# Kernel tuning notes

Measured on AMD Instinct MI355X. Metric: run time of the kernel, lower is better.

## Reference

```python
import jax, jax.numpy as jnp
import numpy as np

N = 100000      # total nodes (herb + ingredient + target concatenated)
E = 1600000     # edges (all etypes concatenated)
D_IN = 128
D_HID = 128
D_OUT = 128
BN_EPS = 1e-5
LEAKY_SLOPE = 0.01


def setup_inputs() -> dict:
    key = jax.random.key(0)
    ks = jax.random.split(key, 8)
    x = jax.random.normal(ks[0], (N, D_IN), dtype=jnp.float32)
    src = jax.random.randint(ks[1], (E,), 0, N, dtype=jnp.int32)
    dst = jax.random.randint(ks[2], (E,), 0, N, dtype=jnp.int32)
    W1 = jax.random.normal(ks[3], (D_IN, D_HID), dtype=jnp.float32) * (1.0 / np.sqrt(D_IN))
    b1 = jnp.zeros((D_HID,), jnp.float32)
    W2 = jax.random.normal(ks[4], (D_HID, D_OUT), dtype=jnp.float32) * (1.0 / np.sqrt(D_HID))
    b2 = jnp.zeros((D_OUT,), jnp.float32)
    gamma = jnp.ones((D_HID,), jnp.float32)
    beta = jnp.zeros((D_HID,), jnp.float32)
    run_mean = jax.random.normal(ks[5], (D_HID,), jnp.float32) * 0.1
    run_var = jax.random.uniform(ks[6], (D_HID,), jnp.float32, 0.5, 1.5)
    return {"x": x, "src": src, "dst": dst, "W1": W1, "b1": b1,
            "W2": W2, "b2": b2, "gamma": gamma, "beta": beta,
            "run_mean": run_mean, "run_var": run_var}


def _graph_conv(h, s, d, W, b, norm_src, norm_dst):
    # DGL GraphConv, norm='both': D_out^{-1/2} then sum-aggregate then D_in^{-1/2}, then linear
    h = h * norm_src                                   # [N, d]
    m = jax.ops.segment_sum(h[s], d, num_segments=N)   # gather + spmm-aggregate
    m = m * norm_dst
    return m @ W + b


def reference(x, src, dst, W1, b1, W2, b2, gamma, beta, run_mean, run_var):
    # dgl.add_self_loop: append (i, i) for every node
    loop = jnp.arange(N, dtype=src.dtype)
    s = jnp.concatenate([src, loop])
    d = jnp.concatenate([dst, loop])
    ones = jnp.ones(s.shape[0], jnp.float32)
    out_deg = jnp.maximum(jax.ops.segment_sum(ones, s, num_segments=N), 1.0)
    in_deg = jnp.maximum(jax.ops.segment_sum(ones, d, num_segments=N), 1.0)
    norm_src = (out_deg ** -0.5)[:, None]
    norm_dst = (in_deg ** -0.5)[:, None]

    # layer 0: conv -> BN (eval, running stats) -> leaky_relu -> dropout (eval = identity)
    h = _graph_conv(x, s, d, W1, b1, norm_src, norm_dst)
    h = (h - run_mean) * jax.lax.rsqrt(run_var + BN_EPS) * gamma + beta
    h = jnp.where(h > 0, h, LEAKY_SLOPE * h)

    # layer 1 (last): conv only
    h = _graph_conv(h, s, d, W2, b2, norm_src, norm_dst)
    return h
```

## Files before the change

kernel.cpp:

```cpp
#include <hip/hip_runtime.h>

#define NN 100000
#define NE 1600000
#define D 128
#define LEAKY 0.01f
#define BNEPS 1e-5f

#define GS 128
#define CHUNK 12500
#define B 782
#define BSHIFT 7
#define BMASK 127
#define NSB (B * GS / 256)

typedef short v8s __attribute__((ext_vector_type(8)));
typedef float v4f __attribute__((ext_vector_type(4)));

__device__ __forceinline__ unsigned f2bf(float f) {
    unsigned u = __float_as_uint(f);
    return (u + 0x7fffu + ((u >> 16) & 1u)) >> 16;
}
__device__ __forceinline__ float bf2f(unsigned h) {
    return __uint_as_float(h << 16);
}


__global__ __launch_bounds__(1024) void hist_kernel(const int* __restrict__ src,
                                                    const int* __restrict__ dst,
                                                    int* __restrict__ hist,
                                                    int* __restrict__ hist2) {
    __shared__ int h[B];
    __shared__ int h2[B];
    for (int i = threadIdx.x; i < B; i += 1024) { h[i] = 0; h2[i] = 0; }
    __syncthreads();
    int g = blockIdx.x;
    const int* dp = dst + g * CHUNK;
    const int* sp = src + g * CHUNK;
    for (int k = threadIdx.x; k < CHUNK; k += 1024) {
        atomicAdd(&h[dp[k] >> BSHIFT], 1);
        atomicAdd(&h2[sp[k] >> BSHIFT], 1);
    }
    __syncthreads();
    for (int i = threadIdx.x; i < B; i += 1024) {
        hist[i * GS + g]  = h[i];
        hist2[i * GS + g] = h2[i];
    }
}

__global__ void scanA2(const int* __restrict__ a, const int* __restrict__ a2,
                       int* __restrict__ bsum, int* __restrict__ bsum2) {
    __shared__ int sm[256];
    int t = threadIdx.x;
    bool second = blockIdx.x >= NSB;
    int blk = second ? blockIdx.x - NSB : blockIdx.x;
    const int* sp = second ? a2 : a;
    sm[t] = sp[blk * 256 + t];
    __syncthreads();
    for (int s = 128; s > 0; s >>= 1) {
        if (t < s) sm[t] += sm[t + s];
        __syncthreads();
    }
    if (t == 0) (second ? bsum2 : bsum)[blk] = sm[0];
}

__global__ void scanC2(const int* __restrict__ a, const int* __restrict__ a2,
                       const int* __restrict__ bsum, const int* __restrict__ bsum2,
                       int* __restrict__ offs, int* __restrict__ offs2) {
    __shared__ int sm[256];
    __shared__ int bo;
    int t = threadIdx.x;
    bool second = blockIdx.x >= NSB;
    int blk = second ? blockIdx.x - NSB : blockIdx.x;
    const int* sp = second ? a2 : a;
    const int* bs = second ? bsum2 : bsum;
    int part = 0;
    for (int j = t; j < blk; j += 256) part += bs[j];
    sm[t] = part;
    __syncthreads();
    for (int s = 128; s > 0; s >>= 1) {
        if (t < s) sm[t] += sm[t + s];
        __syncthreads();
    }
    if (t == 0) bo = sm[0];
    __syncthreads();
    int i = blk * 256 + t;
    int v = sp[i];
    sm[t] = v;
    __syncthreads();
    for (int off = 1; off < 256; off <<= 1) {
        int x = (t >= off) ? sm[t - off] : 0;
        __syncthreads();
        sm[t] += x;
        __syncthreads();
    }
    (second ? offs2 : offs)[i] = bo + sm[t] - v;
}

__global__ __launch_bounds__(1024) void sort_kernel(const int* __restrict__ src,
                                                    const int* __restrict__ dst,
                                                    const int* __restrict__ offs,
                                                    const int* __restrict__ offs2,
                                                    unsigned* __restrict__ ebuf,
                                                    unsigned char* __restrict__ sbuf8) {
    __shared__ int cur[B];
    __shared__ int cur2[B];
    int g = blockIdx.x;
    for (int i = threadIdx.x; i < B; i += 1024) {
        cur[i]  = offs[i * GS + g];
        cur2[i] = offs2[i * GS + g];
    }
    __syncthreads();
    const int* sp = src + g * CHUNK;
    const int* dp = dst + g * CHUNK;
    for (int k = threadIdx.x; k < CHUNK; k += 1024) {
        int d = dp[k], s = sp[k];
        int pos = atomicAdd(&cur[d >> BSHIFT], 1);
        ebuf[pos] = ((unsigned)(d & BMASK) << 17) | (unsigned)s;
        int pos2 = atomicAdd(&cur2[s >> BSHIFT], 1);
        sbuf8[pos2] = (unsigned char)(s & BMASK);
    }
}


__global__ __launch_bounds__(256) void bucket_prep(
    const int* __restrict__ offs, const int* __restrict__ offs2,
    unsigned* __restrict__ ebuf, const unsigned char* __restrict__ sbuf8,
    const float* __restrict__ x, int* __restrict__ row,
    float* __restrict__ norm_s, float* __restrict__ norm_d,
    unsigned* __restrict__ hb)
{
    __shared__ int cnt[128];
    __shared__ int sc[128];
    __shared__ float nsm[128];
    const int b = blockIdx.x;
    const int t = threadIdx.x;

    {
        const int s = offs2[b * GS];
        const int e = (b == B - 1) ? NE : offs2[(b + 1) * GS];
        if (t < 128) cnt[t] = 0;
        __syncthreads();
        for (int k = s + t; k < e; k += 256)
            atomicAdd(&cnt[sbuf8[k]], 1);
        __syncthreads();
        if (t < 128) {
            int node = b * 128 + t;
            if (node < NN) {
                float ns = rsqrtf((float)(cnt[t] + 1));
                norm_s[node] = ns;
                nsm[t] = ns;
            }
        }
        __syncthreads();
        for (int idx = t; idx < 128 * 32; idx += 256) {
            int r = idx >> 5, q = idx & 31;
            int node = b * 128 + r;
            if (node >= NN) continue;
            float ns = nsm[r];
            float4 v = ((const float4*)x)[(size_t)node * 32 + q];
            uint2 w;
            w.x = f2bf(v.x * ns) | (f2bf(v.y * ns) << 16);
            w.y = f2bf(v.z * ns) | (f2bf(v.w * ns) << 16);
            *(uint2*)(hb + (size_t)node * 64 + 2 * q) = w;
        }
    }
    __syncthreads();

    {
        const int s = offs[b * GS];
        const int e = (b == B - 1) ? NE : offs[(b + 1) * GS];
        if (t < 128) cnt[t] = 0;
        __syncthreads();

        unsigned ent[16];
        int nent = 0;
        for (int k = s + t; k < e && nent < 16; k += 256) {
            unsigned u = ebuf[k];
            ent[nent++] = u;
            atomicAdd(&cnt[u >> 17], 1);
        }
        __syncthreads();

        if (t < 128) sc[t] = cnt[t];
        __syncthreads();
        for (int off = 1; off < 128; off <<= 1) {
            int v = 0;
            if (t < 128 && t >= off) v = sc[t - off];
            __syncthreads();
            if (t < 128) sc[t] += v;
            __syncthreads();
        }
        if (t < 128) {
            int st = s + sc[t] - cnt[t];
            int node = b * 128 + t;
            if (node < NN) {
                row[node] = st;
                norm_d[node] = rsqrtf((float)(cnt[t] + 1));
            }
            cnt[t] = st;
        }
        if (b == B - 1 && t == 0) row[NN] = NE;
        __syncthreads();

        for (int i = 0; i < nent; ++i) {
            unsigned u = ent[i];
            int pos = atomicAdd(&cnt[u >> 17], 1);
            ebuf[pos] = u & 0x1FFFFu;
        }
    }
}


__global__ __launch_bounds__(256) void csr_agg(
    const int* __restrict__ rowp, const int* __restrict__ csr,
    const unsigned* __restrict__ hp,
    unsigned* __restrict__ Ahi, unsigned* __restrict__ Alo)
{
    int i = blockIdx.x * 4 + (threadIdx.x >> 6);
    if (i >= NN) return;
    const int lane = threadIdx.x & 63;
    const int half = lane >> 5;
    const int c2   = lane & 31;

    float4 acc = {0.f, 0.f, 0.f, 0.f};
    if (half == 0) {
        uint2 u = *(const uint2*)(hp + (size_t)i * 64 + 2 * c2);
        acc.x = __uint_as_float(u.x << 16);
        acc.y = __uint_as_float(u.x & 0xffff0000u);
        acc.z = __uint_as_float(u.y << 16);
        acc.w = __uint_as_float(u.y & 0xffff0000u);
    }

    int start = rowp[i], end = rowp[i + 1];
    for (int base = start; base < end; base += 64) {
        int n = end - base; if (n > 64) n = 64;
        int sv = csr[base + (lane < n ? lane : n - 1)];
        int nfull = n & ~15;
        int j = 0;
        for (; j < nfull; j += 16) {
            int ss[8]; uint2 uu[8];
            #pragma unroll
            for (int t = 0; t < 8; ++t) ss[t] = __shfl(sv, j + 2 * t + half);
            #pragma unroll
            for (int t = 0; t < 8; ++t)
                uu[t] = *(const uint2*)(hp + (size_t)ss[t] * 64 + 2 * c2);
            #pragma unroll
            for (int t = 0; t < 8; ++t) {
                acc.x += __uint_as_float(uu[t].x << 16);
                acc.y += __uint_as_float(uu[t].x & 0xffff0000u);
                acc.z += __uint_as_float(uu[t].y << 16);
                acc.w += __uint_as_float(uu[t].y & 0xffff0000u);
            }
        }
        if (j < n) {
            int ss[8]; uint2 uu[8];
            #pragma unroll
            for (int t = 0; t < 8; ++t) {
                int e = j + 2 * t + half;
                ss[t] = __shfl(sv, e < n ? e : n - 1);
            }
            #pragma unroll
            for (int t = 0; t < 8; ++t)
                uu[t] = *(const uint2*)(hp + (size_t)ss[t] * 64 + 2 * c2);
            #pragma unroll
            for (int t = 0; t < 8; ++t) {
                if (j + 2 * t + half < n) {
                    acc.x += __uint_as_float(uu[t].x << 16);
                    acc.y += __uint_as_float(uu[t].x & 0xffff0000u);
                    acc.z += __uint_as_float(uu[t].y << 16);
                    acc.w += __uint_as_float(uu[t].y & 0xffff0000u);
                }
            }
        }
    }

    acc.x += __shfl_xor(acc.x, 32);
    acc.y += __shfl_xor(acc.y, 32);
    acc.z += __shfl_xor(acc.z, 32);
    acc.w += __shfl_xor(acc.w, 32);

    unsigned h0 = f2bf(acc.x), h1 = f2bf(acc.y);
    unsigned h2 = f2bf(acc.z), h3 = f2bf(acc.w);
    if (half == 0) {
        uint2 w = { h0 | (h1 << 16), h2 | (h3 << 16) };
        *(uint2*)(Ahi + (size_t)i * 64 + 2 * c2) = w;
    } else {
        float l0 = acc.x - bf2f(h0), l1 = acc.y - bf2f(h1);
        float l2 = acc.z - bf2f(h2), l3 = acc.w - bf2f(h3);
        uint2 w = { f2bf(l0) | (f2bf(l1) << 16), f2bf(l2) | (f2bf(l3) << 16) };
        *(uint2*)(Alo + (size_t)i * 64 + 2 * c2) = w;
    }
}


template<bool LAYER0>
__global__ __launch_bounds__(256) void gemm_kernel(
    const unsigned* __restrict__ Ahi_g, const unsigned* __restrict__ Alo_g,
    const float* __restrict__ W, const float* __restrict__ bias,
    const float* __restrict__ norm_s, const float* __restrict__ norm_d,
    const float* __restrict__ gamma, const float* __restrict__ beta,
    const float* __restrict__ rmean, const float* __restrict__ rvar,
    float* __restrict__ outf, unsigned short* __restrict__ outb)
{
    __shared__ unsigned lhi[64 * 68];
    __shared__ unsigned llo[64 * 68];

    const int w    = threadIdx.x >> 6;
    const int lane = threadIdx.x & 63;
    const int quad = lane >> 4;
    const int l16  = lane & 15;

    v8s Bhi[2][4], Blo[2][4];
    int col[2];
    #pragma unroll
    for (int ct = 0; ct < 2; ++ct) {
        col[ct] = 32 * w + 16 * ct + l16;
        #pragma unroll
        for (int q = 0; q < 4; ++q) {
            int kb = 32 * q + quad * 8;
            v8s hi8, lo8;
            #pragma unroll
            for (int kk = 0; kk < 8; ++kk) {
                float wv = W[(kb + kk) * D + col[ct]];
                unsigned h = f2bf(wv);
                hi8[kk] = (short)h;
                lo8[kk] = (short)f2bf(wv - bf2f(h));
            }
            Bhi[ct][q] = hi8;
            Blo[ct][q] = lo8;
        }
    }

    float bcol[2], s[2] = {0.f, 0.f}, sh[2] = {0.f, 0.f};
    #pragma unroll
    for (int ct = 0; ct < 2; ++ct) {
        bcol[ct] = bias[col[ct]];
        if (LAYER0) {
            s[ct]  = gamma[col[ct]] * rsqrtf(rvar[col[ct]] + BNEPS);
            sh[ct] = beta[col[ct]] - rmean[col[ct]] * s[ct];
        }
    }

    for (int row0 = blockIdx.x * 64; row0 < NN; row0 += gridDim.x * 64) {
        __syncthreads();
        for (int idx = threadIdx.x; idx < 64 * 64; idx += 256) {
            int r = idx >> 6, cp = idx & 63;
            int rw = row0 + r;
            unsigned vh = 0, vl = 0;
            if (rw < NN) {
                vh = Ahi_g[(size_t)rw * 64 + cp];
                vl = Alo_g[(size_t)rw * 64 + cp];
            }
            lhi[r * 68 + cp] = vh;
            llo[r * 68 + cp] = vl;
        }
        __syncthreads();

        #pragma unroll
        for (int rt = 0; rt < 4; ++rt) {
            v4f acc0 = {0.f, 0.f, 0.f, 0.f};
            v4f acc1 = {0.f, 0.f, 0.f, 0.f};
            #pragma unroll
            for (int q = 0; q < 4; ++q) {
                const unsigned short* ph = (const unsigned short*)lhi
                    + (rt * 16 + l16) * 136 + q * 32 + quad * 8;
                const unsigned short* pl = (const unsigned short*)llo
                    + (rt * 16 + l16) * 136 + q * 32 + quad * 8;
                v8s ahi = *(const v8s*)ph;
                v8s alo = *(const v8s*)pl;
                acc0 = __builtin_amdgcn_mfma_f32_16x16x32_bf16(ahi, Bhi[0][q], acc0, 0, 0, 0);
                acc0 = __builtin_amdgcn_mfma_f32_16x16x32_bf16(alo, Bhi[0][q], acc0, 0, 0, 0);
                acc0 = __builtin_amdgcn_mfma_f32_16x16x32_bf16(ahi, Blo[0][q], acc0, 0, 0, 0);
                acc1 = __builtin_amdgcn_mfma_f32_16x16x32_bf16(ahi, Bhi[1][q], acc1, 0, 0, 0);
                acc1 = __builtin_amdgcn_mfma_f32_16x16x32_bf16(alo, Bhi[1][q], acc1, 0, 0, 0);
                acc1 = __builtin_amdgcn_mfma_f32_16x16x32_bf16(ahi, Blo[1][q], acc1, 0, 0, 0);
            }
            #pragma unroll
            for (int r = 0; r < 4; ++r) {
                int rw = row0 + rt * 16 + quad * 4 + r;
                if (rw >= NN) continue;
                float nd = norm_d[rw];
                float o0 = acc0[r] * nd + bcol[0];
                float o1 = acc1[r] * nd + bcol[1];
                if (LAYER0) {
                    o0 = o0 * s[0] + sh[0];
                    o1 = o1 * s[1] + sh[1];
                    o0 = o0 > 0.f ? o0 : LEAKY * o0;
                    o1 = o1 > 0.f ? o1 : LEAKY * o1;
                    float ns = norm_s[rw];
                    o0 *= ns; o1 *= ns;
                    outb[(size_t)rw * D + col[0]] = (unsigned short)f2bf(o0);
                    outb[(size_t)rw * D + col[1]] = (unsigned short)f2bf(o1);
                } else {
                    outf[(size_t)rw * D + col[0]] = o0;
                    outf[(size_t)rw * D + col[1]] = o1;
                }
            }
        }
    }
}


extern "C" void kernel_launch(void* const* d_in, const int* in_sizes, int n_in,
                              void* d_out, int out_size, void* d_ws, size_t ws_size,
                              hipStream_t stream) {
    const float* x     = (const float*)d_in[0];
    const int*   src   = (const int*)d_in[1];
    const int*   dst   = (const int*)d_in[2];
    const float* W1    = (const float*)d_in[3];
    const float* b1    = (const float*)d_in[4];
    const float* W2    = (const float*)d_in[5];
    const float* b2    = (const float*)d_in[6];
    const float* gamma = (const float*)d_in[7];
    const float* beta  = (const float*)d_in[8];
    const float* rmean = (const float*)d_in[9];
    const float* rvar  = (const float*)d_in[10];
    float* out = (float*)d_out;

    unsigned* hb = (unsigned*)d_out;

    unsigned* Ahi   = (unsigned*)d_ws;
    unsigned* Alo   = Ahi + (size_t)NN * 64;
    float*    norm  = (float*)(Alo + (size_t)NN * 64);
    int*      aux   = (int*)(norm + 2 * NN);
    int*      hist  = aux + NN;
    int*      offs  = hist + B * GS;
    int*      bsum  = offs + B * GS;
    int*      boffs = bsum + B;
    unsigned* ebuf  = (unsigned*)(boffs + B);
    float* norm_s = norm;
    float* norm_d = norm + NN;
    int*   row    = hist;
    int*   bsum2  = aux;

    int*           hist2 = (int*)Ahi;
    int*           offs2 = hist2 + B * GS;
    unsigned char* sbuf8 = (unsigned char*)(offs2 + B * GS);

    hist_kernel<<<GS, 1024, 0, stream>>>(src, dst, hist, hist2);
    scanA2<<<2 * NSB, 256, 0, stream>>>(hist, hist2, bsum, bsum2);
    scanC2<<<2 * NSB, 256, 0, stream>>>(hist, hist2, bsum, bsum2, offs, offs2);
    sort_kernel<<<GS, 1024, 0, stream>>>(src, dst, offs, offs2, ebuf, sbuf8);
    bucket_prep<<<B, 256, 0, stream>>>(offs, offs2, ebuf, sbuf8, x, row,
                                       norm_s, norm_d, hb);

    const int AGG_BLOCKS = (NN + 3) / 4;
    const int GEMM_BLOCKS = 784;
    csr_agg<<<AGG_BLOCKS, 256, 0, stream>>>(row, (const int*)ebuf, hb, Ahi, Alo);
    gemm_kernel<true><<<GEMM_BLOCKS, 256, 0, stream>>>(Ahi, Alo, W1, b1,
                                                       norm_s, norm_d,
                                                       gamma, beta, rmean, rvar,
                                                       nullptr, (unsigned short*)hb);
    csr_agg<<<AGG_BLOCKS, 256, 0, stream>>>(row, (const int*)ebuf, hb, Ahi, Alo);
    gemm_kernel<false><<<GEMM_BLOCKS, 256, 0, stream>>>(Ahi, Alo, W2, b2,
                                                        norm_s, norm_d,
                                                        nullptr, nullptr, nullptr, nullptr,
                                                        out, nullptr);
}
```

Baseline: 399.2 us.

## Stage bucket scatter through LDS-local sort for coalesced global writes

The edge bucketing kernel now counts bucket sizes per chunk, builds local prefix sums in shared memory, scatters edges into an LDS buffer, then writes them out to global memory in bucket-contiguous runs located by binary search. The group count is doubled and the chunk halved so the local buffers fit in shared memory. This aims to replace scattered single-element global writes with more contiguous ones. In exchange it adds extra passes, two 1024-wide scans with many barriers, and a binary search per element.

```diff
diff --git a/kernel.cpp b/kernel.cpp
--- a/kernel.cpp
+++ b/kernel.cpp
@@ -6,8 +6,8 @@
 #define LEAKY 0.01f
 #define BNEPS 1e-5f
 
-#define GS 128
-#define CHUNK 12500
+#define GS 256
+#define CHUNK 6250
 #define B 782
 #define BSHIFT 7
 #define BMASK 127
@@ -96,28 +96,83 @@
     (second ? offs2 : offs)[i] = bo + sm[t] - v;
 }
 
+
 __global__ __launch_bounds__(1024) void sort_kernel(const int* __restrict__ src,
                                                     const int* __restrict__ dst,
                                                     const int* __restrict__ offs,
                                                     const int* __restrict__ offs2,
                                                     unsigned* __restrict__ ebuf,
                                                     unsigned char* __restrict__ sbuf8) {
-    __shared__ int cur[B];
+    __shared__ unsigned      lbuf[CHUNK];
+    __shared__ unsigned char lbuf2[CHUNK];
+    __shared__ int lst [B + 1];
+    __shared__ int lst2[B + 1];
+    __shared__ int cur [B];
     __shared__ int cur2[B];
-    int g = blockIdx.x;
-    for (int i = threadIdx.x; i < B; i += 1024) {
-        cur[i]  = offs[i * GS + g];
-        cur2[i] = offs2[i * GS + g];
-    }
-    __syncthreads();
+    __shared__ int ss[1024];
+
+    const int g = blockIdx.x;
+    const int t = threadIdx.x;
     const int* sp = src + g * CHUNK;
     const int* dp = dst + g * CHUNK;
-    for (int k = threadIdx.x; k < CHUNK; k += 1024) {
+
+    for (int i = t; i < B; i += 1024) { cur[i] = 0; cur2[i] = 0; }
+    __syncthreads();
+    for (int k = t; k < CHUNK; k += 1024) {
+        atomicAdd(&cur [dp[k] >> BSHIFT], 1);
+        atomicAdd(&cur2[sp[k] >> BSHIFT], 1);
+    }
+    __syncthreads();
+
+    {
+        int v = (t < B) ? cur[t] : 0;
+        ss[t] = v;
+        __syncthreads();
+        for (int off = 1; off < 1024; off <<= 1) {
+            int x = (t >= off) ? ss[t - off] : 0;
+            __syncthreads();
+            ss[t] += x;
+            __syncthreads();
+        }
+        if (t < B) lst[t] = ss[t] - v;
+        if (t == 0) lst[B] = CHUNK;
+    }
+    __syncthreads();
+    {
+        int v = (t < B) ? cur2[t] : 0;
+        ss[t] = v;
+        __syncthreads();
+        for (int off = 1; off < 1024; off <<= 1) {
+            int x = (t >= off) ? ss[t - off] : 0;
+            __syncthreads();
+            ss[t] += x;
+            __syncthreads();
+        }
+        if (t < B) lst2[t] = ss[t] - v;
+        if (t == 0) lst2[B] = CHUNK;
+    }
+    __syncthreads();
+    for (int i = t; i < B; i += 1024) { cur[i] = lst[i]; cur2[i] = lst2[i]; }
+    __syncthreads();
+
+    for (int k = t; k < CHUNK; k += 1024) {
         int d = dp[k], s = sp[k];
-        int pos = atomicAdd(&cur[d >> BSHIFT], 1);
-        ebuf[pos] = ((unsigned)(d & BMASK) << 17) | (unsigned)s;
-        int pos2 = atomicAdd(&cur2[s >> BSHIFT], 1);
-        sbuf8[pos2] = (unsigned char)(s & BMASK);
+        int p  = atomicAdd(&cur [d >> BSHIFT], 1);
+        lbuf[p] = ((unsigned)(d & BMASK) << 17) | (unsigned)s;
+        int p2 = atomicAdd(&cur2[s >> BSHIFT], 1);
+        lbuf2[p2] = (unsigned char)(s & BMASK);
+    }
+    __syncthreads();
+
+    for (int idx = t; idx < CHUNK; idx += 1024) {
+        int lo = 0, hi = B;
+        while (hi - lo > 1) { int mid = (lo + hi) >> 1; if (lst[mid] <= idx) lo = mid; else hi = mid; }
+        ebuf[offs[lo * GS + g] + (idx - lst[lo])] = lbuf[idx];
+    }
+    for (int idx = t; idx < CHUNK; idx += 1024) {
+        int lo = 0, hi = B;
+        while (hi - lo > 1) { int mid = (lo + hi) >> 1; if (lst2[mid] <= idx) lo = mid; else hi = mid; }
+        sbuf8[offs2[lo * GS + g] + (idx - lst2[lo])] = lbuf2[idx];
     }
 }
 
```

After: 391.5 us. About the same (-1.9%).
